# Kernel tuning notes

Hardware: AMD Instinct MI355X
Metric: run time of the kernel (lower is better)

The kernel has to match this reference:

```python
import jax, jax.numpy as jnp
import numpy as np

B, L, S, H, E = 4, 2048, 2048, 8, 64


def setup_inputs() -> dict:
    key = jax.random.key(0)
    kq, kk, kv, kt = jax.random.split(key, 4)
    queries = jax.random.normal(kq, (B, L, H, E), dtype=jnp.float32)
    keys = jax.random.normal(kk, (B, S, H, E), dtype=jnp.float32)
    values = jax.random.normal(kv, (B, S, H, E), dtype=jnp.float32)
    # de-stationarization log-scale factor, kept small so exp(tau) ~ O(1)
    tau = 0.1 * jax.random.normal(kt, (B, 1, 1, 1), dtype=jnp.float32)
    # causal mask: True above the diagonal (positions to be masked)
    attn_mask = jnp.triu(jnp.ones((L, S), dtype=bool), k=1)
    return {"queries": queries, "keys": keys, "values": values,
            "attn_mask": attn_mask, "tau": tau}


def reference(queries, keys, values, attn_mask, tau):
    # queries: [B,L,H,E], keys/values: [B,S,H,E], tau: [B,1,1,1], mask: [L,S]
    E_ = queries.shape[-1]
    scale = 1.0 / jnp.sqrt(jnp.asarray(E_, dtype=queries.dtype))
    # scores: [B,H,L,S], with tau-based de-stationarization rescale
    scores = jnp.einsum('blhe,bshe->bhls', queries, keys) * (scale * jnp.exp(tau))
    scores = jnp.where(attn_mask, -jnp.inf, scores)
    A = jax.nn.softmax(scores, axis=-1)  # dropout is identity at inference
    V = jnp.einsum('bhls,bshd->blhd', A, values)
    return V
```

## Files before the change

### kernel.cpp

```cpp
#include <hip/hip_runtime.h>
#include <hip/hip_bf16.h>
#include <math.h>

#define B_ 4
#define L_ 2048
#define H_ 8
#define E_ 64
#define HE 512

typedef short bf16x8 __attribute__((ext_vector_type(8)));
typedef float f32x4 __attribute__((ext_vector_type(4)));
typedef float f32x2 __attribute__((ext_vector_type(2)));
typedef unsigned short u16x4 __attribute__((ext_vector_type(4)));
typedef unsigned short u16x8 __attribute__((ext_vector_type(8)));

__device__ __forceinline__ unsigned short f2b(float f) {
  return __builtin_bit_cast(unsigned short, (__hip_bfloat16)f);
}

__global__ __launch_bounds__(512, 4) void attn_fwd(
    const float* __restrict__ Q, const float* __restrict__ K,
    const float* __restrict__ V, const float* __restrict__ tau,
    float* __restrict__ O)
{
  const int f  = blockIdx.x + 16 * (blockIdx.y + 8 * blockIdx.z);
  const int u  = f >> 5, hb = f & 31;
  const int h  = hb & 7, b = hb >> 3;
  const int qt = (u < 8) ? u : 23 - u;

  const int tid  = threadIdx.x;
  const int wave = tid >> 6, lane = tid & 63;
  const int lg = lane >> 4, ll = lane & 15;
  const int llm = ll & 7;

  __shared__ unsigned short ldsK[2][64 * 64];
  __shared__ unsigned short ldsV[2][64 * 64];

  const float qscale = 0.125f * expf(tau[b]) * 1.44269504088896f;
  const int q0w = qt * 128 + wave * 16;

  const float* Qb = Q + (((size_t)b * L_ + (q0w + ll)) * H_ + h) * E_;
  bf16x8 qf[2];
  #pragma unroll
  for (int ek = 0; ek < 2; ++ek) {
    f32x4 a = *(const f32x4*)(Qb + ek * 32 + lg * 8);
    f32x4 c = *(const f32x4*)(Qb + ek * 32 + lg * 8 + 4);
    #pragma unroll
    for (int j = 0; j < 4; ++j) {
      qf[ek][j]     = (short)f2b(a[j] * qscale);
      qf[ek][4 + j] = (short)f2b(c[j] * qscale);
    }
  }

  float m_run = -INFINITY, l_run = 0.0f;
  f32x4 oacc[4];
  #pragma unroll
  for (int n = 0; n < 4; ++n) {
    oacc[n][0] = 0.f; oacc[n][1] = 0.f; oacc[n][2] = 0.f; oacc[n][3] = 0.f;
  }

  const int krow = tid >> 3, kcol = (tid & 7) * 8;
  const int vq = tid >> 5,  vc = (tid & 31) * 2;
  const float* Kp = K + ((size_t)b * L_ * H_ + h) * E_ + (size_t)krow * HE + kcol;
  const float* Vp = V + ((size_t)b * L_ * H_ + h) * E_ + (size_t)(4 * vq) * HE + vc;
  const int kw_off = krow * 64 + (((tid & 7) ^ (krow & 7)) << 3);

  const int nt = 2 * qt + 2;
  const int tmaxw = 2 * qt + (wave >> 2);

  {
    f32x4 k0 = *(const f32x4*)(Kp);
    f32x4 k1 = *(const f32x4*)(Kp + 4);
    f32x2 v0 = *(const f32x2*)(Vp);
    f32x2 v1 = *(const f32x2*)(Vp + HE);
    f32x2 v2 = *(const f32x2*)(Vp + 2 * HE);
    f32x2 v3 = *(const f32x2*)(Vp + 3 * HE);
    u16x8 kw;
    #pragma unroll
    for (int j = 0; j < 4; ++j) { kw[j] = f2b(k0[j]); kw[4 + j] = f2b(k1[j]); }
    *(u16x8*)(&ldsK[0][kw_off]) = kw;
    #pragma unroll
    for (int jj = 0; jj < 2; ++jj) {
      const int row = vc + jj;
      u16x4 vw;
      vw[0] = f2b(v0[jj]); vw[1] = f2b(v1[jj]);
      vw[2] = f2b(v2[jj]); vw[3] = f2b(v3[jj]);
      *(u16x4*)(&ldsV[0][row * 64 + (((vq >> 1) ^ (row & 7)) << 3) + 4 * (vq & 1)]) = vw;
    }
  }
  __syncthreads();
  int cur = 0;

  for (int t = 0; t < nt; ++t) {
    const bool havenext = (t + 1 < nt);
    f32x4 k0, k1; f32x2 v0, v1, v2, v3;
    if (havenext) {
      const float* Kn = Kp + (size_t)(t + 1) * 64 * HE;
      const float* Vn = Vp + (size_t)(t + 1) * 64 * HE;
      k0 = *(const f32x4*)(Kn);
      k1 = *(const f32x4*)(Kn + 4);
      v0 = *(const f32x2*)(Vn);
      v1 = *(const f32x2*)(Vn + HE);
      v2 = *(const f32x2*)(Vn + 2 * HE);
      v3 = *(const f32x2*)(Vn + 3 * HE);
    }

    if (t <= tmaxw) {
      const unsigned short* Kl = ldsK[cur];
      const unsigned short* Vl = ldsV[cur];

      f32x4 sacc[4];
      #pragma unroll
      for (int m = 0; m < 4; ++m) {
        sacc[m][0] = 0.f; sacc[m][1] = 0.f; sacc[m][2] = 0.f; sacc[m][3] = 0.f;
      }
      #pragma unroll
      for (int ek = 0; ek < 2; ++ek) {
        #pragma unroll
        for (int m = 0; m < 4; ++m) {
          bf16x8 kf = *(const bf16x8*)(Kl + (16 * m + ll) * 64 +
                                       ((((ek << 2) + lg) ^ llm) << 3));
          sacc[m] = __builtin_amdgcn_mfma_f32_16x16x32_bf16(kf, qf[ek], sacc[m], 0, 0, 0);
        }
      }

      if (t == tmaxw) {
        const int dq = q0w + ll - 64 * t;
        #pragma unroll
        for (int m = 0; m < 4; ++m)
          #pragma unroll
          for (int r = 0; r < 4; ++r)
            if (16 * m + 4 * lg + r > dq) sacc[m][r] = -3.0e38f;
      }

      float mx = sacc[0][0];
      #pragma unroll
      for (int m = 0; m < 4; ++m)
        #pragma unroll
        for (int r = 0; r < 4; ++r)
          mx = fmaxf(mx, sacc[m][r]);
      mx = fmaxf(mx, __shfl_xor(mx, 16));
      mx = fmaxf(mx, __shfl_xor(mx, 32));
      const float mnew = fmaxf(m_run, mx);
      const float corr = exp2f(m_run - mnew);
      m_run = mnew;
      float rs = 0.0f;
      #pragma unroll
      for (int m = 0; m < 4; ++m)
        #pragma unroll
        for (int r = 0; r < 4; ++r) {
          const float p = exp2f(sacc[m][r] - mnew);
          sacc[m][r] = p;
          rs += p;
        }
      rs += __shfl_xor(rs, 16);
      rs += __shfl_xor(rs, 32);
      l_run = l_run * corr + rs;

      #pragma unroll
      for (int r = 0; r < 4; ++r) {
        const float cr = __shfl(corr, 4 * lg + r);
        #pragma unroll
        for (int n = 0; n < 4; ++n) oacc[n][r] *= cr;
      }

      bf16x8 pf[2];
      #pragma unroll
      for (int ek = 0; ek < 2; ++ek)
        #pragma unroll
        for (int r = 0; r < 4; ++r) {
          pf[ek][r]     = (short)f2b(sacc[2 * ek][r]);
          pf[ek][4 + r] = (short)f2b(sacc[2 * ek + 1][r]);
        }

      #pragma unroll
      for (int ek = 0; ek < 2; ++ek) {
        #pragma unroll
        for (int n = 0; n < 4; ++n) {
          const int d = 16 * n + ll;
          const int base = d * 64 + 4 * (lg & 1);
          u16x4 lo = *(const u16x4*)(Vl + base +
                       ((((ek << 2) + (lg >> 1)) ^ llm) << 3));
          u16x4 hi = *(const u16x4*)(Vl + base +
                       ((((ek << 2) + 2 + (lg >> 1)) ^ llm) << 3));
          bf16x8 vf;
          #pragma unroll
          for (int i = 0; i < 4; ++i) {
            vf[i]     = (short)lo[i];
            vf[4 + i] = (short)hi[i];
          }
          oacc[n] = __builtin_amdgcn_mfma_f32_16x16x32_bf16(pf[ek], vf, oacc[n], 0, 0, 0);
        }
      }
    }

    if (havenext) {
      const int nb = cur ^ 1;
      u16x8 kw;
      #pragma unroll
      for (int j = 0; j < 4; ++j) { kw[j] = f2b(k0[j]); kw[4 + j] = f2b(k1[j]); }
      *(u16x8*)(&ldsK[nb][kw_off]) = kw;
      #pragma unroll
      for (int jj = 0; jj < 2; ++jj) {
        const int row = vc + jj;
        u16x4 vw;
        vw[0] = f2b(v0[jj]); vw[1] = f2b(v1[jj]);
        vw[2] = f2b(v2[jj]); vw[3] = f2b(v3[jj]);
        *(u16x4*)(&ldsV[nb][row * 64 + (((vq >> 1) ^ (row & 7)) << 3) + 4 * (vq & 1)]) = vw;
      }
      __syncthreads();
      cur = nb;
    }
  }

  const float linv = 1.0f / l_run;
  float* Ob = O + (((size_t)b * L_ + q0w) * H_ + h) * E_;
  #pragma unroll
  for (int r = 0; r < 4; ++r) {
    const float inv = __shfl(linv, 4 * lg + r);
    const int qrow = 4 * lg + r;
    #pragma unroll
    for (int n = 0; n < 4; ++n)
      Ob[(size_t)qrow * HE + 16 * n + ll] = oacc[n][r] * inv;
  }
}

extern "C" void kernel_launch(void* const* d_in, const int* in_sizes, int n_in,
                              void* d_out, int out_size, void* d_ws, size_t ws_size,
                              hipStream_t stream) {
  (void)in_sizes; (void)n_in; (void)out_size; (void)d_ws; (void)ws_size;
  const float* Q   = (const float*)d_in[0];
  const float* K   = (const float*)d_in[1];
  const float* V   = (const float*)d_in[2];
  const float* tau = (const float*)d_in[4];
  float* O = (float*)d_out;
  dim3 grid(L_ / 128, H_, B_), block(512);
  hipLaunchKernelGGL(attn_fwd, grid, block, 0, stream, Q, K, V, tau, O);
}
```

Before: 58.53 us.

## Skip lazy softmax rescale, add MFMA priority hints, tree-reduce max/sum

Applies a lazy online-softmax rescale: the running max and the output/denominator correction happen only when some lane's new max exceeds the running max by more than 8 (log2 units), otherwise the old max is reused. Also wraps both MFMA loops in s_setprio to favour matrix issue across waves, turns the row max and sum into balanced trees, and builds the V fragment through a union instead of element copies. The aim is to cut the per-tile exp/shuffle/rescale VALU work. The trade is exponentials up to 2^8 before bf16 conversion, which stays safe in fp32 range.

```diff
diff --git a/kernel.cpp b/kernel.cpp
--- a/kernel.cpp
+++ b/kernel.cpp
@@ -59,9 +59,9 @@
     oacc[n][0] = 0.f; oacc[n][1] = 0.f; oacc[n][2] = 0.f; oacc[n][3] = 0.f;
   }
 
-  const int krow = tid >> 3, kcol = (tid & 7) * 8;
+  const int krow = tid >> 3;
   const int vq = tid >> 5,  vc = (tid & 31) * 2;
-  const float* Kp = K + ((size_t)b * L_ * H_ + h) * E_ + (size_t)krow * HE + kcol;
+  const float* Kp = K + ((size_t)b * L_ * H_ + h) * E_ + (size_t)krow * HE + (tid & 7) * 8;
   const float* Vp = V + ((size_t)b * L_ * H_ + h) * E_ + (size_t)(4 * vq) * HE + vc;
   const int kw_off = krow * 64 + (((tid & 7) ^ (krow & 7)) << 3);
 
@@ -114,6 +114,7 @@
       for (int m = 0; m < 4; ++m) {
         sacc[m][0] = 0.f; sacc[m][1] = 0.f; sacc[m][2] = 0.f; sacc[m][3] = 0.f;
       }
+      __builtin_amdgcn_s_setprio(1);
       #pragma unroll
       for (int ek = 0; ek < 2; ++ek) {
         #pragma unroll
@@ -123,6 +124,7 @@
           sacc[m] = __builtin_amdgcn_mfma_f32_16x16x32_bf16(kf, qf[ek], sacc[m], 0, 0, 0);
         }
       }
+      __builtin_amdgcn_s_setprio(0);
 
       if (t == tmaxw) {
         const int dq = q0w + ll - 64 * t;
@@ -133,36 +135,41 @@
             if (16 * m + 4 * lg + r > dq) sacc[m][r] = -3.0e38f;
       }
 
-      float mx = sacc[0][0];
-      #pragma unroll
-      for (int m = 0; m < 4; ++m)
-        #pragma unroll
-        for (int r = 0; r < 4; ++r)
-          mx = fmaxf(mx, sacc[m][r]);
+      float t0 = fmaxf(fmaxf(sacc[0][0], sacc[0][1]), fmaxf(sacc[0][2], sacc[0][3]));
+      float t1 = fmaxf(fmaxf(sacc[1][0], sacc[1][1]), fmaxf(sacc[1][2], sacc[1][3]));
+      float t2 = fmaxf(fmaxf(sacc[2][0], sacc[2][1]), fmaxf(sacc[2][2], sacc[2][3]));
+      float t3 = fmaxf(fmaxf(sacc[3][0], sacc[3][1]), fmaxf(sacc[3][2], sacc[3][3]));
+      float mx = fmaxf(fmaxf(t0, t1), fmaxf(t2, t3));
       mx = fmaxf(mx, __shfl_xor(mx, 16));
       mx = fmaxf(mx, __shfl_xor(mx, 32));
-      const float mnew = fmaxf(m_run, mx);
-      const float corr = exp2f(m_run - mnew);
-      m_run = mnew;
-      float rs = 0.0f;
+
+      if (!__all(mx - m_run <= 8.0f)) {
+        const float mnew = fmaxf(m_run, mx);
+        const float corr = exp2f(m_run - mnew);
+        m_run = mnew;
+        l_run *= corr;
+        #pragma unroll
+        for (int r = 0; r < 4; ++r) {
+          const float cr = __shfl(corr, 4 * lg + r);
+          #pragma unroll
+          for (int n = 0; n < 4; ++n) oacc[n][r] *= cr;
+        }
+      }
+
       #pragma unroll
       for (int m = 0; m < 4; ++m)
         #pragma unroll
-        for (int r = 0; r < 4; ++r) {
-          const float p = exp2f(sacc[m][r] - mnew);
-          sacc[m][r] = p;
-          rs += p;
-        }
+        for (int r = 0; r < 4; ++r)
+          sacc[m][r] = exp2f(sacc[m][r] - m_run);
+
+      float s0 = (sacc[0][0] + sacc[0][1]) + (sacc[0][2] + sacc[0][3]);
+      float s1 = (sacc[1][0] + sacc[1][1]) + (sacc[1][2] + sacc[1][3]);
+      float s2 = (sacc[2][0] + sacc[2][1]) + (sacc[2][2] + sacc[2][3]);
+      float s3 = (sacc[3][0] + sacc[3][1]) + (sacc[3][2] + sacc[3][3]);
+      float rs = (s0 + s1) + (s2 + s3);
       rs += __shfl_xor(rs, 16);
       rs += __shfl_xor(rs, 32);
-      l_run = l_run * corr + rs;
-
-      #pragma unroll
-      for (int r = 0; r < 4; ++r) {
-        const float cr = __shfl(corr, 4 * lg + r);
-        #pragma unroll
-        for (int n = 0; n < 4; ++n) oacc[n][r] *= cr;
-      }
+      l_run += rs;
 
       bf16x8 pf[2];
       #pragma unroll
@@ -173,25 +180,22 @@
           pf[ek][4 + r] = (short)f2b(sacc[2 * ek + 1][r]);
         }
 
+      __builtin_amdgcn_s_setprio(1);
       #pragma unroll
       for (int ek = 0; ek < 2; ++ek) {
         #pragma unroll
         for (int n = 0; n < 4; ++n) {
           const int d = 16 * n + ll;
           const int base = d * 64 + 4 * (lg & 1);
-          u16x4 lo = *(const u16x4*)(Vl + base +
+          union { bf16x8 v8; u16x4 q[2]; } vu;
+          vu.q[0] = *(const u16x4*)(Vl + base +
                        ((((ek << 2) + (lg >> 1)) ^ llm) << 3));
-          u16x4 hi = *(const u16x4*)(Vl + base +
+          vu.q[1] = *(const u16x4*)(Vl + base +
                        ((((ek << 2) + 2 + (lg >> 1)) ^ llm) << 3));
-          bf16x8 vf;
-          #pragma unroll
-          for (int i = 0; i < 4; ++i) {
-            vf[i]     = (short)lo[i];
-            vf[4 + i] = (short)hi[i];
-          }
-          oacc[n] = __builtin_amdgcn_mfma_f32_16x16x32_bf16(pf[ek], vf, oacc[n], 0, 0, 0);
-        }
-      }
+          oacc[n] = __builtin_amdgcn_mfma_f32_16x16x32_bf16(pf[ek], vu.v8, oacc[n], 0, 0, 0);
+        }
+      }
+      __builtin_amdgcn_s_setprio(0);
     }
 
     if (havenext) {
```

Measured after the change: 60.26 us. +3.0%, slower.
